# Kernel tuning notes

Measured on AMD Instinct MI355X. Metric: run time of the kernel, lower is better.

The kernel has to match this reference:

```python
import jax, jax.numpy as jnp
import numpy as np

D_MODEL = 1024
H = 16
D_K = D_MODEL // H


def setup_inputs() -> dict:
    key = jax.random.key(0)
    ks = jax.random.split(key, 9)
    s = 0.02
    x = jax.random.normal(ks[0], (2, 2048, D_MODEL), dtype=jnp.float32)
    Wq = jax.random.normal(ks[1], (D_MODEL, D_MODEL), dtype=jnp.float32) * s
    bq = jax.random.normal(ks[2], (D_MODEL,), dtype=jnp.float32) * s
    Wk = jax.random.normal(ks[3], (D_MODEL, D_MODEL), dtype=jnp.float32) * s
    bk = jax.random.normal(ks[4], (D_MODEL,), dtype=jnp.float32) * s
    Wv = jax.random.normal(ks[5], (D_MODEL, D_MODEL), dtype=jnp.float32) * s
    bv = jax.random.normal(ks[6], (D_MODEL,), dtype=jnp.float32) * s
    Wo = jax.random.normal(ks[7], (D_MODEL, D_MODEL), dtype=jnp.float32) * s
    bo = jax.random.normal(ks[8], (D_MODEL,), dtype=jnp.float32) * s
    return {"x": x, "Wq": Wq, "bq": bq, "Wk": Wk, "bk": bk,
            "Wv": Wv, "bv": bv, "Wo": Wo, "bo": bo}


def reference(x, Wq, bq, Wk, bk, Wv, bv, Wo, bo):
    b, s, _ = x.shape
    scale = 1.0 / jnp.sqrt(jnp.float32(D_K))
    # projections; [b, s, d] -> [b, h, s, d_k]
    def split_heads(t):
        return t.reshape(b, s, H, D_K).transpose(0, 2, 1, 3)
    q = split_heads(x @ Wq + bq)
    k = split_heads(x @ Wk + bk)
    v = split_heads(x @ Wv + bv)
    scores = jnp.einsum('bhqd,bhkd->bhqk', q, k) * scale  # [b,h,s,s]
    attn = jax.nn.softmax(scores, axis=-1)
    ctx = jnp.einsum('bhqk,bhkd->bhqd', attn, v)
    ctx = ctx.transpose(0, 2, 1, 3).reshape(b, s, D_MODEL)
    return ctx @ Wo + bo + x
```

## Files before the change

kernel.cpp:

```cpp
#include <hip/hip_runtime.h>
#include <hip/hip_bf16.h>
#include <stdint.h>

#define D_MODEL 1024
#define NH 16
#define DK 64
#define S_LEN 2048

typedef __attribute__((ext_vector_type(8))) __bf16 bf16x8;
typedef __attribute__((ext_vector_type(4))) float f32x4;

#define GLOBAL_AS __attribute__((address_space(1)))
#define LDS_AS    __attribute__((address_space(3)))

__device__ __forceinline__ void async16(const ushort* g, ushort* l) {
    __builtin_amdgcn_global_load_lds(
        (const GLOBAL_AS uint32_t*)(uintptr_t)(const void*)g,
        (LDS_AS uint32_t*)(uint32_t)(uintptr_t)(void*)l,
        16, 0, 0);
}

template <int N>
__device__ __forceinline__ void pipe_barrier() {
    asm volatile("s_waitcnt vmcnt(%0)\n\ts_barrier" :: "n"(N) : "memory");
}

__device__ __forceinline__ float fast_exp2(float x) {
    float r;
    asm("v_exp_f32 %0, %1" : "=v"(r) : "v"(x));
    return r;
}

__device__ __forceinline__ ushort f2bf(float f) {
    union { float f; uint32_t u; } v; v.f = f;
    uint32_t lsb = (v.u >> 16) & 1u;
    return (ushort)((v.u + 0x7fffu + lsb) >> 16);
}

__device__ __forceinline__ uint32_t packbf(float a, float b) {
    union { float f; uint32_t u; } x, y; x.f = a; y.f = b;
    return ((x.u + 0x8000u) >> 16) | ((y.u + 0x8000u) & 0xffff0000u);
}

__device__ __forceinline__ bf16x8 ldfrag(const ushort* p) {
    union { uint4 u; bf16x8 b; } cv;
    cv.u = *(const uint4*)p;
    return cv.b;
}


__global__ void cvt_x_kernel(const float* __restrict__ x, ushort* __restrict__ xb) {
    int i = blockIdx.x * 256 + threadIdx.x;
    float4 v = ((const float4*)x)[i];
    ushort4 o;
    o.x = f2bf(v.x); o.y = f2bf(v.y); o.z = f2bf(v.z); o.w = f2bf(v.w);
    ((ushort4*)xb)[i] = o;
}

__global__ void transpose_cvt4_kernel(
    const float* __restrict__ W0, const float* __restrict__ W1,
    const float* __restrict__ W2, const float* __restrict__ W3,
    ushort* __restrict__ D0, ushort* __restrict__ D1,
    ushort* __restrict__ D2, ushort* __restrict__ D3) {
    const float* W; ushort* D;
    switch (blockIdx.z) {
        case 0: W = W0; D = D0; break;
        case 1: W = W1; D = D1; break;
        case 2: W = W2; D = D2; break;
        default: W = W3; D = D3; break;
    }
    __shared__ float tile[32][33];
    int bx = blockIdx.x * 32, by = blockIdx.y * 32;
    int tx = threadIdx.x, ty = threadIdx.y;
#pragma unroll
    for (int j = 0; j < 32; j += 8)
        tile[ty + j][tx] = W[(size_t)(by + ty + j) * D_MODEL + bx + tx];
    __syncthreads();
#pragma unroll
    for (int j = 0; j < 32; j += 8)
        D[(size_t)(bx + ty + j) * D_MODEL + by + tx] = f2bf(tile[tx][ty + j]);
}

__global__ void cvt_bias_kernel(const float* __restrict__ bq, const float* __restrict__ bk,
                                const float* __restrict__ bv, float* __restrict__ out) {
    int i = blockIdx.x * 256 + threadIdx.x;
    float v = (i < 1024) ? bq[i] : (i < 2048 ? bk[i - 1024] : bv[i - 2048]);
    out[i] = v;
}

template <int MODE>
__global__ __launch_bounds__(256) void gemm_kernel(
    const ushort* __restrict__ A, const ushort* __restrict__ Bt,
    const float* __restrict__ bias,
    ushort* __restrict__ outQ, ushort* __restrict__ outK, ushort* __restrict__ outVt,
    const float* __restrict__ xres, float* __restrict__ outF) {
    constexpr int BN = (MODE == 0) ? 128 : 64;
    constexpr int NI = (MODE == 0) ? 4 : 2;
    constexpr int NS = (MODE == 0) ? 4 : 3;
    __shared__ __align__(16) ushort sA[3][128 * 32];
    __shared__ __align__(16) ushort sB[3][BN * 32];
    const int tid = threadIdx.x;
    const int wave = tid >> 6, lane = tid & 63;
    const int lr = lane & 15, lq = lane >> 4;
    const int srow = lane >> 2;
    const int sc = (lane & 3) ^ ((lane >> 4) & 3);

    const int bid = blockIdx.x;
    const int xcd = bid & 7, lb = bid >> 3;
    int bx, by;
    if (MODE == 0) { bx = xcd * 3 + (lb % 3); by = lb / 3; }
    else           { by = xcd * 4 + (lb & 3); bx = lb >> 2; }
    const int blockM = by * 128;
    const int blockN = bx * BN;
    const int waveM = (wave >> 1) * 64;
    const int waveN = (MODE == 0) ? (wave & 1) * 64 : (wave & 1) * 32;

    auto stage = [&](int k0, ushort* a, ushort* b) {
#pragma unroll
        for (int t = 0; t < 2; t++) {
            int row = wave * 32 + t * 16 + srow;
            async16(&A[(size_t)(blockM + row) * D_MODEL + k0 + sc * 8],
                    &a[(wave * 32 + t * 16) * 32]);
        }
        if (MODE == 0) {
#pragma unroll
            for (int t = 0; t < 2; t++) {
                int row = wave * 32 + t * 16 + srow;
                async16(&Bt[(size_t)(blockN + row) * D_MODEL + k0 + sc * 8],
                        &b[(wave * 32 + t * 16) * 32]);
            }
        } else {
            int row = wave * 16 + srow;
            async16(&Bt[(size_t)(blockN + row) * D_MODEL + k0 + sc * 8],
                    &b[wave * 16 * 32]);
        }
    };

    f32x4 acc[4][NI] = {};
    const int swz = (lq ^ ((lr >> 2) & 3)) * 8;

    stage(0, sA[0], sB[0]);
    stage(32, sA[1], sB[1]);
    __syncthreads();

    int cur = 0;
#pragma unroll 4
    for (int k = 0; k < 32; k++) {
        int nx = cur + 2; if (nx >= 3) nx -= 3;
        if (k + 2 < 32) stage((k + 2) * 32, sA[nx], sB[nx]);
        const ushort* a = sA[cur];
        const ushort* b = sB[cur];
        bf16x8 af[4], bfr[NI];
#pragma unroll
        for (int mi = 0; mi < 4; mi++)
            af[mi] = ldfrag(&a[(waveM + mi * 16 + lr) * 32 + swz]);
#pragma unroll
        for (int ni = 0; ni < NI; ni++)
            bfr[ni] = ldfrag(&b[(waveN + ni * 16 + lr) * 32 + swz]);
#pragma unroll
        for (int mi = 0; mi < 4; mi++)
#pragma unroll
            for (int ni = 0; ni < NI; ni++)
                acc[mi][ni] = __builtin_amdgcn_mfma_f32_16x16x32_bf16(
                    af[mi], bfr[ni], acc[mi][ni], 0, 0, 0);
        if (k < 30) pipe_barrier<NS>();
        else if (k == 30) pipe_barrier<0>();
        cur = (cur == 2) ? 0 : cur + 1;
    }

#pragma unroll
    for (int mi = 0; mi < 4; mi++) {
#pragma unroll
        for (int ni = 0; ni < NI; ni++) {
#pragma unroll
            for (int r = 0; r < 4; r++) {
                int m = blockM + waveM + mi * 16 + lq * 4 + r;
                int n = blockN + waveN + ni * 16 + lr;
                float v = acc[mi][ni][r] + bias[n];
                if (MODE == 0) {
                    int which = n >> 10, c = n & 1023;
                    int h = c >> 6, d = c & 63;
                    int b2 = m >> 11, s = m & 2047;
                    size_t bh = (size_t)(b2 * NH + h);
                    if (which == 0)
                        outQ[(bh * S_LEN + s) * DK + d] = f2bf(v * 0.1803368801f);
                    else if (which == 1)
                        outK[(bh * S_LEN + s) * DK + d] = f2bf(v);
                    else
                        outVt[(bh * DK + d) * S_LEN + s] = f2bf(v);
                } else {
                    size_t idx = (size_t)m * D_MODEL + n;
                    outF[idx] = v + xres[idx];
                }
            }
        }
    }
}

__global__ __launch_bounds__(256, 4) void attn_kernel(
    const ushort* __restrict__ Q, const ushort* __restrict__ Km,
    const ushort* __restrict__ Vt, ushort* __restrict__ ctx) {
    const int bid = blockIdx.x;
    const int xcd = bid & 7, lb = bid >> 3;
    const int bh = xcd * 4 + (lb & 3);
    const int qt = lb >> 2;
    const int q0 = qt * 64;
    __shared__ __align__(16) ushort sQP[4][16 * 64];
    __shared__ __align__(16) ushort sK[64 * 64];
    __shared__ __align__(16) ushort sV[64 * 64];
    const int tid = threadIdx.x;
    const int wave = tid >> 6, lane = tid & 63;
    const int lr = lane & 15, lq = lane >> 4;
    const int srow = lane >> 3, sp = lane & 7;
    const ushort* Qh = Q + (size_t)bh * S_LEN * DK;
    const ushort* Kh = Km + (size_t)bh * S_LEN * DK;
    const ushort* Vh = Vt + (size_t)bh * DK * S_LEN;
    ushort* sPw = sQP[wave];

#pragma unroll
    for (int t = 0; t < 2; t++) {
        int row = t * 8 + srow;
        int c = sp ^ (row & 7);
        async16(&Qh[(size_t)(q0 + wave * 16 + row) * DK + c * 8],
                &sPw[t * 8 * 64]);
    }
    __syncthreads();

    bf16x8 qf[2];
#pragma unroll
    for (int kk = 0; kk < 2; kk++)
        qf[kk] = ldfrag(&sPw[lr * 64 + (((kk * 4 + lq) ^ (lr & 7)) * 8)]);

    union { uint4 u; bf16x8 b; } one_u;
    one_u.u = make_uint4(0x3F803F80u, 0x3F803F80u, 0x3F803F80u, 0x3F803F80u);
    const bf16x8 ones = one_u.b;

    f32x4 cacc[4] = {};
    f32x4 ssum = {};

    for (int k0 = 0; k0 < S_LEN; k0 += 64) {
        __syncthreads();
#pragma unroll
        for (int t = 0; t < 2; t++) {
            int row = wave * 16 + t * 8 + srow;
            int c = sp ^ (row & 7);
            async16(&Kh[(size_t)(k0 + row) * DK + c * 8], &sK[(wave * 16 + t * 8) * 64]);
            async16(&Vh[(size_t)row * S_LEN + k0 + c * 8], &sV[(wave * 16 + t * 8) * 64]);
        }
        __syncthreads();

        f32x4 sacc[4] = {};
#pragma unroll
        for (int kk = 0; kk < 2; kk++) {
            int swz = ((kk * 4 + lq) ^ (lr & 7)) * 8;
#pragma unroll
            for (int nj = 0; nj < 4; nj++) {
                bf16x8 kf = ldfrag(&sK[(nj * 16 + lr) * 64 + swz]);
                sacc[nj] = __builtin_amdgcn_mfma_f32_16x16x32_bf16(
                    kf, qf[kk], sacc[nj], 0, 0, 0);
            }
        }

#pragma unroll
        for (int nj = 0; nj < 4; nj++) {
            float p0 = fast_exp2(sacc[nj][0]);
            float p1 = fast_exp2(sacc[nj][1]);
            float p2 = fast_exp2(sacc[nj][2]);
            float p3 = fast_exp2(sacc[nj][3]);
            uint2 w;
            w.x = packbf(p0, p1);
            w.y = packbf(p2, p3);
            int physc = (nj * 2 + (lq >> 1)) ^ (lr & 7);
            *(uint2*)&sPw[lr * 64 + physc * 8 + (lq & 1) * 4] = w;
        }

#pragma unroll
        for (int ks = 0; ks < 2; ks++) {
            bf16x8 pf = ldfrag(&sPw[lr * 64 + (((ks * 4 + lq) ^ (lr & 7)) * 8)]);
            int swz = ((ks * 4 + lq) ^ (lr & 7)) * 8;
#pragma unroll
            for (int nd = 0; nd < 4; nd++) {
                bf16x8 vf = ldfrag(&sV[(nd * 16 + lr) * 64 + swz]);
                cacc[nd] = __builtin_amdgcn_mfma_f32_16x16x32_bf16(
                    pf, vf, cacc[nd], 0, 0, 0);
            }
            ssum = __builtin_amdgcn_mfma_f32_16x16x32_bf16(pf, ones, ssum, 0, 0, 0);
        }
    }

    const int b = bh >> 4, h = bh & 15;
    float inv[4];
#pragma unroll
    for (int r = 0; r < 4; r++) inv[r] = __builtin_amdgcn_rcpf(ssum[r]);
#pragma unroll
    for (int nd = 0; nd < 4; nd++)
#pragma unroll
        for (int r = 0; r < 4; r++) {
            int qrow = q0 + wave * 16 + lq * 4 + r;
            int d = nd * 16 + lr;
            float v = cacc[nd][r] * inv[r];
            ctx[(size_t)(b * S_LEN + qrow) * D_MODEL + h * DK + d] = f2bf(v);
        }
}


extern "C" void kernel_launch(void* const* d_in, const int* in_sizes, int n_in,
                              void* d_out, int out_size, void* d_ws, size_t ws_size,
                              hipStream_t stream) {
    const float* x  = (const float*)d_in[0];
    const float* Wq = (const float*)d_in[1];
    const float* bq = (const float*)d_in[2];
    const float* Wk = (const float*)d_in[3];
    const float* bk = (const float*)d_in[4];
    const float* Wv = (const float*)d_in[5];
    const float* bv = (const float*)d_in[6];
    const float* Wo = (const float*)d_in[7];
    const float* bo = (const float*)d_in[8];

    char* ws = (char*)d_ws;
    ushort* xb    = (ushort*)(ws);
    ushort* wqkv  = (ushort*)(ws + (8ull  << 20));
    ushort* wo_t  = (ushort*)(ws + (14ull << 20));
    ushort* qbuf  = (ushort*)(ws + (16ull << 20));
    ushort* kbuf  = (ushort*)(ws + (24ull << 20));
    ushort* vtb   = (ushort*)(ws + (32ull << 20));
    ushort* ctx   = (ushort*)(ws + (40ull << 20));
    float*  biasq = (float*)(ws + (48ull << 20));

    cvt_x_kernel<<<4096, 256, 0, stream>>>(x, xb);
    transpose_cvt4_kernel<<<dim3(32, 32, 4), dim3(32, 8), 0, stream>>>(
        Wq, Wk, Wv, Wo, wqkv, wqkv + 1024 * 1024, wqkv + 2 * 1024 * 1024, wo_t);
    cvt_bias_kernel<<<12, 256, 0, stream>>>(bq, bk, bv, biasq);

    gemm_kernel<0><<<768, 256, 0, stream>>>(
        xb, wqkv, biasq, qbuf, kbuf, vtb, nullptr, nullptr);
    attn_kernel<<<1024, 256, 0, stream>>>(qbuf, kbuf, vtb, ctx);
    gemm_kernel<1><<<512, 256, 0, stream>>>(
        ctx, wo_t, bo, nullptr, nullptr, nullptr, x, (float*)d_out);
}
```

Measured before the change: 217.6 us.

## Triple-buffer K/V loads and double query rows per wave in attention

The attention kernel now handles 128 query rows per block (32 per wave), so each K/V tile loaded into LDS is reused across twice as many queries. K/V staging moves to a three-slot ring buffer that prefetches two tiles ahead, with a single vmcnt-counted barrier per iteration in place of two syncthreads. The grid is halved and launch bounds lowered to 2 blocks per SM, which lowers occupancy and raises register pressure in exchange for more reuse and better overlap of loads with compute.

```diff
diff --git a/kernel.cpp b/kernel.cpp
--- a/kernel.cpp
+++ b/kernel.cpp
@@ -197,17 +197,17 @@
     }
 }
 
-__global__ __launch_bounds__(256, 4) void attn_kernel(
+__global__ __launch_bounds__(256, 2) void attn_kernel(
     const ushort* __restrict__ Q, const ushort* __restrict__ Km,
     const ushort* __restrict__ Vt, ushort* __restrict__ ctx) {
     const int bid = blockIdx.x;
     const int xcd = bid & 7, lb = bid >> 3;
     const int bh = xcd * 4 + (lb & 3);
     const int qt = lb >> 2;
-    const int q0 = qt * 64;
-    __shared__ __align__(16) ushort sQP[4][16 * 64];
-    __shared__ __align__(16) ushort sK[64 * 64];
-    __shared__ __align__(16) ushort sV[64 * 64];
+    const int q0 = qt * 128;
+    __shared__ __align__(16) ushort sK[3][64 * 64];
+    __shared__ __align__(16) ushort sV[3][64 * 64];
+    __shared__ __align__(16) ushort sQP[4][32 * 64];
     const int tid = threadIdx.x;
     const int wave = tid >> 6, lane = tid & 63;
     const int lr = lane & 15, lq = lane >> 4;
@@ -218,89 +218,127 @@
     ushort* sPw = sQP[wave];
 
 #pragma unroll
-    for (int t = 0; t < 2; t++) {
+    for (int t = 0; t < 4; t++) {
         int row = t * 8 + srow;
         int c = sp ^ (row & 7);
-        async16(&Qh[(size_t)(q0 + wave * 16 + row) * DK + c * 8],
+        async16(&Qh[(size_t)(q0 + wave * 32 + row) * DK + c * 8],
                 &sPw[t * 8 * 64]);
     }
+
+    auto stageKV = [&](int k0, int buf) {
+#pragma unroll
+        for (int t = 0; t < 2; t++) {
+            int row = wave * 16 + t * 8 + srow;
+            int c = sp ^ (row & 7);
+            async16(&Kh[(size_t)(k0 + row) * DK + c * 8],
+                    &sK[buf][(wave * 16 + t * 8) * 64]);
+            async16(&Vh[(size_t)row * S_LEN + k0 + c * 8],
+                    &sV[buf][(wave * 16 + t * 8) * 64]);
+        }
+    };
+
+    stageKV(0, 0);
+    stageKV(64, 1);
     __syncthreads();
 
-    bf16x8 qf[2];
-#pragma unroll
-    for (int kk = 0; kk < 2; kk++)
-        qf[kk] = ldfrag(&sPw[lr * 64 + (((kk * 4 + lq) ^ (lr & 7)) * 8)]);
+    bf16x8 qf[2][2];
+#pragma unroll
+    for (int nj = 0; nj < 2; nj++)
+#pragma unroll
+        for (int kk = 0; kk < 2; kk++)
+            qf[nj][kk] = ldfrag(&sPw[(nj * 16 + lr) * 64 +
+                                     (((kk * 4 + lq) ^ (lr & 7)) * 8)]);
 
     union { uint4 u; bf16x8 b; } one_u;
     one_u.u = make_uint4(0x3F803F80u, 0x3F803F80u, 0x3F803F80u, 0x3F803F80u);
     const bf16x8 ones = one_u.b;
 
-    f32x4 cacc[4] = {};
-    f32x4 ssum = {};
-
-    for (int k0 = 0; k0 < S_LEN; k0 += 64) {
-        __syncthreads();
-#pragma unroll
-        for (int t = 0; t < 2; t++) {
-            int row = wave * 16 + t * 8 + srow;
-            int c = sp ^ (row & 7);
-            async16(&Kh[(size_t)(k0 + row) * DK + c * 8], &sK[(wave * 16 + t * 8) * 64]);
-            async16(&Vh[(size_t)row * S_LEN + k0 + c * 8], &sV[(wave * 16 + t * 8) * 64]);
-        }
-        __syncthreads();
-
-        f32x4 sacc[4] = {};
+    f32x4 cacc[2][4] = {};
+    f32x4 ssum[2] = {};
+
+    int cur = 0;
+    for (int k = 0; k < 32; k++) {
+        int nx = cur + 2; if (nx >= 3) nx -= 3;
+        if (k + 2 < 32) stageKV((k + 2) * 64, nx);
+        const ushort* sk = sK[cur];
+        const ushort* sv = sV[cur];
+
+        f32x4 sacc[4][2] = {};
 #pragma unroll
         for (int kk = 0; kk < 2; kk++) {
+            bf16x8 kf[4];
             int swz = ((kk * 4 + lq) ^ (lr & 7)) * 8;
 #pragma unroll
-            for (int nj = 0; nj < 4; nj++) {
-                bf16x8 kf = ldfrag(&sK[(nj * 16 + lr) * 64 + swz]);
-                sacc[nj] = __builtin_amdgcn_mfma_f32_16x16x32_bf16(
-                    kf, qf[kk], sacc[nj], 0, 0, 0);
+            for (int mi = 0; mi < 4; mi++)
+                kf[mi] = ldfrag(&sk[(mi * 16 + lr) * 64 + swz]);
+#pragma unroll
+            for (int mi = 0; mi < 4; mi++)
+#pragma unroll
+                for (int nj = 0; nj < 2; nj++)
+                    sacc[mi][nj] = __builtin_amdgcn_mfma_f32_16x16x32_bf16(
+                        kf[mi], qf[nj][kk], sacc[mi][nj], 0, 0, 0);
+        }
+
+#pragma unroll
+        for (int mi = 0; mi < 4; mi++)
+#pragma unroll
+            for (int nj = 0; nj < 2; nj++) {
+                float p0 = fast_exp2(sacc[mi][nj][0]);
+                float p1 = fast_exp2(sacc[mi][nj][1]);
+                float p2 = fast_exp2(sacc[mi][nj][2]);
+                float p3 = fast_exp2(sacc[mi][nj][3]);
+                uint2 w;
+                w.x = packbf(p0, p1);
+                w.y = packbf(p2, p3);
+                int physc = (mi * 2 + (lq >> 1)) ^ (lr & 7);
+                *(uint2*)&sPw[(nj * 16 + lr) * 64 + physc * 8 + (lq & 1) * 4] = w;
             }
-        }
-
-#pragma unroll
-        for (int nj = 0; nj < 4; nj++) {
-            float p0 = fast_exp2(sacc[nj][0]);
-            float p1 = fast_exp2(sacc[nj][1]);
-            float p2 = fast_exp2(sacc[nj][2]);
-            float p3 = fast_exp2(sacc[nj][3]);
-            uint2 w;
-            w.x = packbf(p0, p1);
-            w.y = packbf(p2, p3);
-            int physc = (nj * 2 + (lq >> 1)) ^ (lr & 7);
-            *(uint2*)&sPw[lr * 64 + physc * 8 + (lq & 1) * 4] = w;
-        }
 
 #pragma unroll
         for (int ks = 0; ks < 2; ks++) {
-            bf16x8 pf = ldfrag(&sPw[lr * 64 + (((ks * 4 + lq) ^ (lr & 7)) * 8)]);
+            bf16x8 pf[2], vf[4];
             int swz = ((ks * 4 + lq) ^ (lr & 7)) * 8;
 #pragma unroll
-            for (int nd = 0; nd < 4; nd++) {
-                bf16x8 vf = ldfrag(&sV[(nd * 16 + lr) * 64 + swz]);
-                cacc[nd] = __builtin_amdgcn_mfma_f32_16x16x32_bf16(
-                    pf, vf, cacc[nd], 0, 0, 0);
+            for (int nj = 0; nj < 2; nj++)
+                pf[nj] = ldfrag(&sPw[(nj * 16 + lr) * 64 + swz]);
+#pragma unroll
+            for (int nd = 0; nd < 4; nd++)
+                vf[nd] = ldfrag(&sv[(nd * 16 + lr) * 64 + swz]);
+#pragma unroll
+            for (int nj = 0; nj < 2; nj++)
+#pragma unroll
+                for (int nd = 0; nd < 4; nd++)
+                    cacc[nj][nd] = __builtin_amdgcn_mfma_f32_16x16x32_bf16(
+                        pf[nj], vf[nd], cacc[nj][nd], 0, 0, 0);
+#pragma unroll
+            for (int nj = 0; nj < 2; nj++)
+                ssum[nj] = __builtin_amdgcn_mfma_f32_16x16x32_bf16(
+                    pf[nj], ones, ssum[nj], 0, 0, 0);
+        }
+
+        if (k < 30) pipe_barrier<4>();
+        else if (k == 30) pipe_barrier<0>();
+        cur = (cur == 2) ? 0 : cur + 1;
+    }
+
+    const int b = bh >> 4, h = bh & 15;
+    float inv[2][4];
+#pragma unroll
+    for (int nj = 0; nj < 2; nj++)
+#pragma unroll
+        for (int r = 0; r < 4; r++)
+            inv[nj][r] = __builtin_amdgcn_rcpf(ssum[nj][r]);
+#pragma unroll
+    for (int nj = 0; nj < 2; nj++)
+#pragma unroll
+        for (int nd = 0; nd < 4; nd++)
+#pragma unroll
+            for (int r = 0; r < 4; r++) {
+                int qrow = q0 + wave * 32 + nj * 16 + lq * 4 + r;
+                int d = nd * 16 + lr;
+                float v = cacc[nj][nd][r] * inv[nj][r];
+                ctx[(size_t)(b * S_LEN + qrow) * D_MODEL + h * DK + d] = f2bf(v);
             }
-            ssum = __builtin_amdgcn_mfma_f32_16x16x32_bf16(pf, ones, ssum, 0, 0, 0);
-        }
-    }
-
-    const int b = bh >> 4, h = bh & 15;
-    float inv[4];
-#pragma unroll
-    for (int r = 0; r < 4; r++) inv[r] = __builtin_amdgcn_rcpf(ssum[r]);
-#pragma unroll
-    for (int nd = 0; nd < 4; nd++)
-#pragma unroll
-        for (int r = 0; r < 4; r++) {
-            int qrow = q0 + wave * 16 + lq * 4 + r;
-            int d = nd * 16 + lr;
-            float v = cacc[nd][r] * inv[r];
-            ctx[(size_t)(b * S_LEN + qrow) * D_MODEL + h * DK + d] = f2bf(v);
-        }
 }
 
 
@@ -334,7 +372,7 @@
 
     gemm_kernel<0><<<768, 256, 0, stream>>>(
         xb, wqkv, biasq, qbuf, kbuf, vtb, nullptr, nullptr);
-    attn_kernel<<<1024, 256, 0, stream>>>(qbuf, kbuf, vtb, ctx);
+    attn_kernel<<<512, 256, 0, stream>>>(qbuf, kbuf, vtb, ctx);
     gemm_kernel<1><<<512, 256, 0, stream>>>(
         ctx, wo_t, bo, nullptr, nullptr, nullptr, x, (float*)d_out);
 }
```

Result: faster. 211.9 us (-2.6%).
